# Kernel tuning notes

Measured on AMD Instinct MI355X. Metric: run time of the kernel, lower is better.

## Reference

```python
import jax, jax.numpy as jnp
import numpy as np

KS = 3
K3 = KS ** 3
NUM_K = 4
KM_ITERS = 10  # fixed Lloyd iterations (original runs to tolerance)


def _unfold3d(xp, d, h, w):
    # xp: [B, C, d+2, h+2, w+2] -> [B, C, d, h, w, 27]; kernel dims flattened as (k1,k2,k3)
    sl = [xp[:, :, i:i + d, j:j + h, l:l + w]
          for i in range(KS) for j in range(KS) for l in range(KS)]
    return jnp.stack(sl, axis=-1)


def _kmeans(pts):
    # pts: [N, C]. Deterministic init with first NUM_K points, fixed Lloyd iterations.
    cent0 = pts[:NUM_K]

    def assign(cent):
        d2 = (jnp.sum(pts * pts, -1, keepdims=True)
              - 2.0 * (pts @ cent.T) + jnp.sum(cent * cent, -1))  # [N, K]
        return jnp.argmin(d2, axis=-1)

    def step(cent, _):
        oh = jax.nn.one_hot(assign(cent), NUM_K, dtype=pts.dtype)  # [N, K]
        cnt = jnp.maximum(oh.sum(0), 1.0)
        cent = (oh.T @ pts) / cnt[:, None]
        return cent, None

    cent, _ = jax.lax.scan(step, cent0, None, length=KM_ITERS)
    return assign(cent), cent


def _mlp3(z, w1, b1, w2, b2, w3, b3):
    z = jax.nn.relu(z @ w1 + b1)
    z = jax.nn.relu(z @ w2 + b2)
    return z @ w3 + b3


def reference(x, proj_w, base_w, gk_w1, gk_b1, gk_w2, gk_b2, gk_w3, gk_b3,
              gb_w1, gb_b1, gb_w2, gb_b2, gb_w3, gb_b3, prelu_a):
    b, c, d, h, w = x.shape
    o = base_w.shape[0]
    n = d * h * w
    x_in = x
    # 1x1x1 input projection (no bias)
    xp = jnp.einsum('oi,bidhw->bodhw', proj_w, x)
    xp = jnp.pad(xp, ((0, 0), (0, 0), (1, 1), (1, 1), (1, 1)))
    patches = _unfold3d(xp, d, h, w)                                # [b,c,d,h,w,27]
    # mean_type 's': mean over kernel dims -> per-voxel channel summary
    x_mean = patches.mean(-1).reshape(b, c, n).transpose(0, 2, 1)   # [b,n,c]
    idx, cent = jax.vmap(_kmeans)(x_mean)                           # [b,n], [b,K,c]
    feat = cent.reshape(b, NUM_K * c)
    # per-cluster dynamic kernel gates in (0,1)
    w_i = jax.nn.sigmoid(_mlp3(feat, gk_w1, gk_b1, gk_w2, gk_b2, gk_w3, gk_b3))
    w_i = w_i.reshape(b, NUM_K, K3).transpose(1, 0, 2)[:, :, None, None, :]  # [K,b,1,1,27]
    weight = (w_i * base_w).reshape(NUM_K, b, o, c * K3)            # [K,b,o,c*27]
    bias = _mlp3(feat, gb_w1, gb_b1, gb_w2, gb_b2, gb_w3, gb_b3)
    bias = bias.reshape(b, NUM_K, o).transpose(1, 0, 2)[..., None]  # [K,b,o,1]
    # im2col: [b, c*27, n] with (c, k) channel-major flattening as in the torch rearrange
    xf = patches.reshape(b, c, n, K3).transpose(0, 1, 3, 2).reshape(b, c * K3, n)
    out = jnp.einsum('kbof,bfn->kbon', weight, xf) + bias           # [K,b,o,n]
    mask = jax.nn.one_hot(idx, NUM_K, dtype=out.dtype)              # [b,n,K]
    out = (out * mask.transpose(2, 0, 1)[:, :, None, :]).sum(0)     # [b,o,n]
    out = out.reshape(b, o, d, h, w)
    out = jnp.where(out >= 0, out, prelu_a * out)                   # PReLU (single param)
    return out + x_in


def setup_inputs():
    key = jax.random.key(0)
    ks = jax.random.split(key, 12)
    B, C, O, D = 1, 64, 64, 40
    inner, inner2 = 128, 64
    fin = C * NUM_K

    def lin(k, i, o_):
        s = 1.0 / np.sqrt(i)
        return jax.random.uniform(k, (i, o_), jnp.float32, -s, s)

    return {
        'x': jax.random.normal(ks[0], (B, C, D, D, D), jnp.float32),
        'proj_w': jax.random.normal(ks[1], (C, C), jnp.float32) / np.sqrt(C),
        'base_w': jax.random.normal(ks[2], (O, C, K3), jnp.float32) / np.sqrt(C * K3),
        'gk_w1': lin(ks[3], fin, inner), 'gk_b1': jnp.zeros((inner,), jnp.float32),
        'gk_w2': lin(ks[4], inner, inner), 'gk_b2': jnp.zeros((inner,), jnp.float32),
        'gk_w3': lin(ks[5], inner, K3 * NUM_K), 'gk_b3': jnp.zeros((K3 * NUM_K,), jnp.float32),
        'gb_w1': lin(ks[6], fin, inner2), 'gb_b1': jnp.zeros((inner2,), jnp.float32),
        'gb_w2': lin(ks[7], inner2, inner2), 'gb_b2': jnp.zeros((inner2,), jnp.float32),
        'gb_w3': lin(ks[8], inner2, O * NUM_K), 'gb_b3': jnp.zeros((O * NUM_K,), jnp.float32),
        'prelu_a': jnp.full((1,), 0.25, jnp.float32),
    }
```

## Files before the change

### kernel.cpp

```cpp
#include <hip/hip_runtime.h>
#include <math.h>

typedef short v8s __attribute__((ext_vector_type(8)));
typedef float v4f __attribute__((ext_vector_type(4)));

#define NVOX 64000
#define NPAD 74088
#define P2   1764
#define GSTR 592704
#define NCPY 32
#define ITST (NCPY*260)

__device__ __forceinline__ unsigned short bf16rne(float f){
  unsigned int u = __float_as_uint(f);
  u += 0x7FFFu + ((u >> 16) & 1u);
  return (unsigned short)(u >> 16);
}

__global__ __launch_bounds__(256) void proj_k(const float* __restrict__ x,
                                              const float* __restrict__ pw,
                                              float* __restrict__ xp,
                                              short* __restrict__ xpt){
  int tid = threadIdx.x;
  int m = (blockIdx.x >> 1) * 256 + tid;
  int half = blockIdx.x & 1;
  float xv[64];
#pragma unroll
  for (int i = 0; i < 64; i++) xv[i] = x[(size_t)i * NVOX + m];
  int d = m / 1600; int r = m - d * 1600; int h = r / 40; int w = r - h * 40;
  int p = ((d + 1) * 42 + (h + 1)) * 42 + (w + 1);
  const float4* pw4 = (const float4*)pw;
  for (int g8 = half * 4; g8 < half * 4 + 4; g8++){
    v8s pk;
#pragma unroll
    for (int j = 0; j < 8; j++){
      int co = g8 * 8 + j;
      float acc = 0.f;
#pragma unroll
      for (int q = 0; q < 16; q++){
        float4 pv = pw4[co * 16 + q];
        acc = fmaf(pv.x, xv[4*q+0], acc);
        acc = fmaf(pv.y, xv[4*q+1], acc);
        acc = fmaf(pv.z, xv[4*q+2], acc);
        acc = fmaf(pv.w, xv[4*q+3], acc);
      }
      xp[(size_t)co * NVOX + m] = acc;
      pk[j] = (short)bf16rne(acc);
    }
    *(v8s*)(xpt + (size_t)g8 * GSTR + (size_t)p * 8) = pk;
  }
}

__global__ __launch_bounds__(256) void boxwh_k(const float* __restrict__ in,
                                               float* __restrict__ out){
  __shared__ float s0[1600], s1[1600];
  size_t base = (size_t)blockIdx.x * 1600;
  int t = threadIdx.x;
  for (int e = t; e < 1600; e += 256) s0[e] = in[base + e];
  __syncthreads();
  for (int e = t; e < 1600; e += 256){
    int w = e % 40;
    float s = s0[e];
    if (w > 0)  s += s0[e - 1];
    if (w < 39) s += s0[e + 1];
    s1[e] = s;
  }
  __syncthreads();
  for (int e = t; e < 1600; e += 256){
    int h = e / 40;
    float s = s1[e];
    if (h > 0)  s += s1[e - 40];
    if (h < 39) s += s1[e + 40];
    out[base + e] = s;
  }
}
__global__ void boxd_k(const float* __restrict__ in, float* __restrict__ out){
  int g = blockIdx.x * 256 + threadIdx.x;
  int d = (g / 1600) % 40;
  float s = in[g];
  if (d > 0)  s += in[g - 1600];
  if (d < 39) s += in[g + 1600];
  out[g] = s * (1.f / 27.f);
}

__global__ __launch_bounds__(256) void transp_k(const float* __restrict__ in,
                                                float* __restrict__ out,
                                                float* __restrict__ km){
  __shared__ float tile[64][65];
  int t = threadIdx.x;
  int nb = blockIdx.x * 64;
  int l = t & 63, g = t >> 6;
  for (int cc = g; cc < 64; cc += 4)
    tile[cc][l] = in[(size_t)cc * NVOX + nb + l];
  __syncthreads();
  if (blockIdx.x == 0){
    km[t] = tile[t & 63][t >> 6];
    if (t < 4) km[256 + t] = 1.f;
  }
  for (int nn = g; nn < 64; nn += 4)
    out[(size_t)(nb + nn) * 64 + l] = tile[l][nn];
}

__global__ __launch_bounds__(256) void assign_k(const float* __restrict__ xmt,
                                                const float* __restrict__ kin,
                                                float* __restrict__ kout,
                                                int* __restrict__ idx, int mode){
  __shared__ float s_cent[256];
  __shared__ float s_cc[4];
  __shared__ float s_red[260];
  __shared__ float s_x[256 * 65];
  __shared__ int   s_kb[256];
  int t = threadIdx.x, lane = t & 63, wv = t >> 6;
  int n = blockIdx.x * 256 + t;
  {
    float sum = 0.f, cnt = 0.f;
#pragma unroll
    for (int s = 0; s < NCPY; s++){
      sum += kin[s * 260 + t];
      cnt += kin[s * 260 + 256 + (t >> 6)];
    }
    s_cent[t] = sum / fmaxf(cnt, 1.f);
  }
  for (int j = t; j < 260; j += 256) s_red[j] = 0.f;
  __syncthreads();
  if (t < 4){
    const float4* cc4 = (const float4*)(s_cent + t * 64);
    float s = 0.f;
#pragma unroll
    for (int q = 0; q < 16; q++){
      float4 v = cc4[q];
      s = fmaf(v.x, v.x, s); s = fmaf(v.y, v.y, s);
      s = fmaf(v.z, v.z, s); s = fmaf(v.w, v.w, s);
    }
    s_cc[t] = s;
  }
  __syncthreads();
  const float4* xt = (const float4*)(xmt + (size_t)n * 64);
  float4 xq[16];
#pragma unroll
  for (int q = 0; q < 16; q++) xq[q] = xt[q];
  float d0 = 0.f, d1 = 0.f, d2 = 0.f, d3 = 0.f;
  const float4* c4 = (const float4*)s_cent;
#pragma unroll
  for (int q = 0; q < 16; q++){
    float4 p0 = c4[q], p1 = c4[16 + q], p2 = c4[32 + q], p3 = c4[48 + q];
    d0 = fmaf(p0.x, xq[q].x, d0); d0 = fmaf(p0.y, xq[q].y, d0);
    d0 = fmaf(p0.z, xq[q].z, d0); d0 = fmaf(p0.w, xq[q].w, d0);
    d1 = fmaf(p1.x, xq[q].x, d1); d1 = fmaf(p1.y, xq[q].y, d1);
    d1 = fmaf(p1.z, xq[q].z, d1); d1 = fmaf(p1.w, xq[q].w, d1);
    d2 = fmaf(p2.x, xq[q].x, d2); d2 = fmaf(p2.y, xq[q].y, d2);
    d2 = fmaf(p2.z, xq[q].z, d2); d2 = fmaf(p2.w, xq[q].w, d2);
    d3 = fmaf(p3.x, xq[q].x, d3); d3 = fmaf(p3.y, xq[q].y, d3);
    d3 = fmaf(p3.z, xq[q].z, d3); d3 = fmaf(p3.w, xq[q].w, d3);
  }
  float sc0 = s_cc[0] - 2.f * d0;
  float sc1 = s_cc[1] - 2.f * d1;
  float sc2 = s_cc[2] - 2.f * d2;
  float sc3 = s_cc[3] - 2.f * d3;
  int kb = 0; float bs = sc0;
  if (sc1 < bs){ bs = sc1; kb = 1; }
  if (sc2 < bs){ bs = sc2; kb = 2; }
  if (sc3 < bs){ bs = sc3; kb = 3; }
  if (mode){
    idx[n] = kb;
    return;
  }
  s_kb[t] = kb;
#pragma unroll
  for (int q = 0; q < 16; q++){
    s_x[t * 65 + 4*q + 0] = xq[q].x;
    s_x[t * 65 + 4*q + 1] = xq[q].y;
    s_x[t * 65 + 4*q + 2] = xq[q].z;
    s_x[t * 65 + 4*q + 3] = xq[q].w;
  }
  __syncthreads();
  float a0 = 0.f, a1 = 0.f, a2 = 0.f, a3 = 0.f;
  int rowbase = wv * 64;
#pragma unroll 16
  for (int j = 0; j < 64; j++){
    float v = s_x[(rowbase + j) * 65 + lane];
    int kj = s_kb[rowbase + j];
    a0 += (kj == 0) ? v : 0.f;
    a1 += (kj == 1) ? v : 0.f;
    a2 += (kj == 2) ? v : 0.f;
    a3 += (kj == 3) ? v : 0.f;
  }
  atomicAdd(&s_red[lane], a0);
  atomicAdd(&s_red[64 + lane], a1);
  atomicAdd(&s_red[128 + lane], a2);
  atomicAdd(&s_red[192 + lane], a3);
#pragma unroll
  for (int kk = 0; kk < 4; kk++){
    unsigned long long m = __ballot(kb == kk);
    if (lane == 0) atomicAdd(&s_red[256 + kk], (float)__popcll(m));
  }
  __syncthreads();
  float* kslot = kout + (blockIdx.x & (NCPY - 1)) * 260;
  for (int j = t; j < 260; j += 256) atomicAdd(&kslot[j], s_red[j]);
}

__global__ void mlp_k(const float* __restrict__ km10,
                      const float* __restrict__ w1, const float* __restrict__ b1,
                      const float* __restrict__ w2, const float* __restrict__ b2,
                      const float* __restrict__ w3, const float* __restrict__ b3,
                      const float* __restrict__ u1, const float* __restrict__ c1,
                      const float* __restrict__ u2, const float* __restrict__ c2,
                      const float* __restrict__ u3, const float* __restrict__ c3,
                      float* __restrict__ wi, float* __restrict__ bias){
  __shared__ float s_feat[256], s_h1[128], s_h2[128], s_g1[64], s_g2[64];
  int t = threadIdx.x;
  {
    float sum = 0.f, cnt = 0.f;
#pragma unroll
    for (int s = 0; s < NCPY; s++){
      sum += km10[s * 260 + t];
      cnt += km10[s * 260 + 256 + (t >> 6)];
    }
    s_feat[t] = sum / fmaxf(cnt, 1.f);
  }
  __syncthreads();
  if (t < 128){
    float z = b1[t];
    for (int i = 0; i < 256; i++) z = fmaf(s_feat[i], w1[i * 128 + t], z);
    s_h1[t] = fmaxf(z, 0.f);
  }
  __syncthreads();
  if (t < 128){
    float z = b2[t];
    for (int i = 0; i < 128; i++) z = fmaf(s_h1[i], w2[i * 128 + t], z);
    s_h2[t] = fmaxf(z, 0.f);
  }
  __syncthreads();
  if (t < 108){
    float z = b3[t];
    for (int i = 0; i < 128; i++) z = fmaf(s_h2[i], w3[i * 108 + t], z);
    wi[t] = 1.f / (1.f + expf(-z));
  }
  if (t < 64){
    float z = c1[t];
    for (int i = 0; i < 256; i++) z = fmaf(s_feat[i], u1[i * 64 + t], z);
    s_g1[t] = fmaxf(z, 0.f);
  }
  __syncthreads();
  if (t < 64){
    float z = c2[t];
    for (int i = 0; i < 64; i++) z = fmaf(s_g1[i], u2[i * 64 + t], z);
    s_g2[t] = fmaxf(z, 0.f);
  }
  __syncthreads();
  {
    float z = c3[t];
    for (int i = 0; i < 64; i++) z = fmaf(s_g2[i], u3[i * 256 + t], z);
    bias[t] = z;
  }
}

__global__ void bwprep_k(const float* __restrict__ bw, short* __restrict__ bwb){
  int e = blockIdx.x * 256 + threadIdx.x;
  int t = e >> 12; int rem = e & 4095;
  int o = rem >> 6; int c = rem & 63;
  bwb[e] = (short)bf16rne(bw[(o * 64 + c) * 27 + t]);
}

__global__ __launch_bounds__(256) void conv_k(const short* __restrict__ xpt,
                                              const short* __restrict__ bwb,
                                              const float* __restrict__ wi,
                                              const float* __restrict__ bias,
                                              const int* __restrict__ idx,
                                              const float* __restrict__ x,
                                              const float* __restrict__ pa,
                                              float* __restrict__ out){
  static const int POFF[27] = {
    -P2-42-1, -P2-42, -P2-42+1, -P2-1, -P2, -P2+1, -P2+42-1, -P2+42, -P2+42+1,
    -42-1, -42, -42+1, -1, 0, 1, 42-1, 42, 42+1,
    P2-42-1, P2-42, P2-42+1, P2-1, P2, P2+1, P2+42-1, P2+42, P2+42+1 };
  __shared__ float s_wi[108];
  __shared__ float s_bias[256];
  __shared__ float s_acc[64 * 68];
  int tid = threadIdx.x;
  for (int j = tid; j < 108; j += 256) s_wi[j] = wi[j];
  s_bias[tid] = bias[tid];
  __syncthreads();
  int wv = tid >> 6, lane = tid & 63;
  int kc = wv & 1, mh = wv >> 1;
  int col = lane & 15, kg = lane >> 4;
  int vb = blockIdx.x * 64;
  int p4[4], ki4[4];
#pragma unroll
  for (int nt = 0; nt < 4; nt++){
    int v = vb + nt * 16 + col;
    ki4[nt] = idx[v];
    int d = v / 1600; int r = v - d * 1600; int h = r / 40; int w = r - h * 40;
    p4[nt] = ((d + 1) * 42 + (h + 1)) * 42 + (w + 1);
  }
  const short* bg = xpt + (size_t)(kc * 4 + kg) * GSTR;
  const short* bp0 = bg + (size_t)p4[0] * 8;
  const short* bp1 = bg + (size_t)p4[1] * 8;
  const short* bp2 = bg + (size_t)p4[2] * 8;
  const short* bp3 = bg + (size_t)p4[3] * 8;
  int ao0 = (mh * 32 + col) * 64 + kc * 32 + kg * 8;
  int ao1 = ao0 + 16 * 64;
  v4f acc[2][4];
#pragma unroll
  for (int m2 = 0; m2 < 2; m2++)
#pragma unroll
    for (int nt = 0; nt < 4; nt++) acc[m2][nt] = (v4f){0.f, 0.f, 0.f, 0.f};
  v4f zero = {0.f, 0.f, 0.f, 0.f};
#pragma unroll 9
  for (int t = 0; t < 27; t++){
    int po8 = POFF[t] * 8;
    v8s a0 = *(const v8s*)(bwb + t * 4096 + ao0);
    v8s a1 = *(const v8s*)(bwb + t * 4096 + ao1);
    v8s b0 = *(const v8s*)(bp0 + po8);
    v8s b1 = *(const v8s*)(bp1 + po8);
    v8s b2 = *(const v8s*)(bp2 + po8);
    v8s b3 = *(const v8s*)(bp3 + po8);
    float wk0 = s_wi[ki4[0] * 27 + t];
    float wk1 = s_wi[ki4[1] * 27 + t];
    float wk2 = s_wi[ki4[2] * 27 + t];
    float wk3 = s_wi[ki4[3] * 27 + t];
    v4f tp;
    tp = __builtin_amdgcn_mfma_f32_16x16x32_bf16(a0, b0, zero, 0, 0, 0); acc[0][0] += tp * wk0;
    tp = __builtin_amdgcn_mfma_f32_16x16x32_bf16(a1, b0, zero, 0, 0, 0); acc[1][0] += tp * wk0;
    tp = __builtin_amdgcn_mfma_f32_16x16x32_bf16(a0, b1, zero, 0, 0, 0); acc[0][1] += tp * wk1;
    tp = __builtin_amdgcn_mfma_f32_16x16x32_bf16(a1, b1, zero, 0, 0, 0); acc[1][1] += tp * wk1;
    tp = __builtin_amdgcn_mfma_f32_16x16x32_bf16(a0, b2, zero, 0, 0, 0); acc[0][2] += tp * wk2;
    tp = __builtin_amdgcn_mfma_f32_16x16x32_bf16(a1, b2, zero, 0, 0, 0); acc[1][2] += tp * wk2;
    tp = __builtin_amdgcn_mfma_f32_16x16x32_bf16(a0, b3, zero, 0, 0, 0); acc[0][3] += tp * wk3;
    tp = __builtin_amdgcn_mfma_f32_16x16x32_bf16(a1, b3, zero, 0, 0, 0); acc[1][3] += tp * wk3;
  }
  __syncthreads();
  if (kc == 1){
#pragma unroll
    for (int m2 = 0; m2 < 2; m2++)
#pragma unroll
      for (int nt = 0; nt < 4; nt++)
        *(v4f*)(&s_acc[(nt * 16 + col) * 68 + mh * 32 + m2 * 16 + kg * 4]) = acc[m2][nt];
  }
  __syncthreads();
  if (kc == 0){
    float pav = pa[0];
#pragma unroll
    for (int m2 = 0; m2 < 2; m2++){
#pragma unroll
      for (int nt = 0; nt < 4; nt++){
        v4f other = *(const v4f*)(&s_acc[(nt * 16 + col) * 68 + mh * 32 + m2 * 16 + kg * 4]);
        v4f sum = acc[m2][nt] + other;
        int n = vb + nt * 16 + col;
#pragma unroll
        for (int r = 0; r < 4; r++){
          int o = mh * 32 + m2 * 16 + kg * 4 + r;
          float val = sum[r] + s_bias[ki4[nt] * 64 + o];
          val = (val >= 0.f) ? val : pav * val;
          size_t off = (size_t)o * NVOX + n;
          out[off] = val + x[off];
        }
      }
    }
  }
}

extern "C" void kernel_launch(void* const* d_in, const int* in_sizes, int n_in,
                              void* d_out, int out_size, void* d_ws, size_t ws_size,
                              hipStream_t stream){
  const float* x    = (const float*)d_in[0];
  const float* pw   = (const float*)d_in[1];
  const float* bw   = (const float*)d_in[2];
  const float* gkw1 = (const float*)d_in[3];
  const float* gkb1 = (const float*)d_in[4];
  const float* gkw2 = (const float*)d_in[5];
  const float* gkb2 = (const float*)d_in[6];
  const float* gkw3 = (const float*)d_in[7];
  const float* gkb3 = (const float*)d_in[8];
  const float* gbw1 = (const float*)d_in[9];
  const float* gbb1 = (const float*)d_in[10];
  const float* gbw2 = (const float*)d_in[11];
  const float* gbb2 = (const float*)d_in[12];
  const float* gbw3 = (const float*)d_in[13];
  const float* gbb3 = (const float*)d_in[14];
  const float* pa   = (const float*)d_in[15];
  float* outp = (float*)d_out;

  float* ws   = (float*)d_ws;
  float* XP   = ws;
  float* BU2  = ws + 4096000;
  float* BU1  = ws + 8192000;
  short* XPT  = (short*)(ws + 12288000);
  short* BWB  = XPT + (size_t)NPAD * 64;
  float* KM   = (float*)(BWB + 110592);
  float* WI   = KM + 11 * ITST;
  float* BIAS = WI + 108;
  int*   IDX  = (int*)(BIAS + 256);
  float* XMT  = XP;

  hipMemsetAsync(XPT, 0, (size_t)NPAD * 64 * 2, stream);
  hipMemsetAsync(KM, 0, (size_t)11 * ITST * sizeof(float), stream);
  proj_k<<<500, 256, 0, stream>>>(x, pw, XP, XPT);
  boxwh_k<<<2560, 256, 0, stream>>>(XP, BU2);
  boxd_k<<<16000, 256, 0, stream>>>(BU2, BU1);
  transp_k<<<1000, 256, 0, stream>>>(BU1, XMT, KM);
  for (int i = 0; i <= 10; i++)
    assign_k<<<250, 256, 0, stream>>>(XMT, KM + i * ITST, KM + (i + 1) * ITST, IDX,
                                      (i == 10) ? 1 : 0);
  mlp_k<<<1, 256, 0, stream>>>(KM + 10 * ITST,
                               gkw1, gkb1, gkw2, gkb2, gkw3, gkb3,
                               gbw1, gbb1, gbw2, gbb2, gbw3, gbb3,
                               WI, BIAS);
  bwprep_k<<<432, 256, 0, stream>>>(bw, BWB);
  conv_k<<<1000, 256, 0, stream>>>(XPT, BWB, WI, BIAS, IDX, x, pa, outp);
}
```

Before: 322.5 us.

## Fuse k-means iterations into one persistent kernel with grid-wide barrier

Replaces the eleven separate assign_k launches with a single persistent kernel that loops over Lloyd iterations and synchronizes all 250 blocks via a two-level atomic counter barrier. Each block keeps its point data in registers and shared memory across iterations instead of reloading it every launch. This removes per-launch overhead and repeated global reads of the point matrix. It relies on all 250 blocks being co-resident and adds spin-wait barrier latency plus coherent loads of the partial sums.

```diff
diff --git a/kernel.cpp b/kernel.cpp
--- a/kernel.cpp
+++ b/kernel.cpp
@@ -15,6 +15,10 @@
   unsigned int u = __float_as_uint(f);
   u += 0x7FFFu + ((u >> 16) & 1u);
   return (unsigned short)(u >> 16);
+}
+
+__device__ __forceinline__ float cohload(const float* p){
+  return __hip_atomic_load(p, __ATOMIC_RELAXED, __HIP_MEMORY_SCOPE_AGENT);
 }
 
 __global__ __launch_bounds__(256) void proj_k(const float* __restrict__ x,
@@ -101,10 +105,11 @@
     out[(size_t)(nb + nn) * 64 + l] = tile[l][nn];
 }
 
-__global__ __launch_bounds__(256) void assign_k(const float* __restrict__ xmt,
-                                                const float* __restrict__ kin,
-                                                float* __restrict__ kout,
-                                                int* __restrict__ idx, int mode){
+__global__ __launch_bounds__(256) void kmeansp_k(const float* __restrict__ xmt,
+                                                 float* __restrict__ km,
+                                                 int* __restrict__ gcnt,
+                                                 int* __restrict__ gmast,
+                                                 int* __restrict__ idx){
   __shared__ float s_cent[256];
   __shared__ float s_cc[4];
   __shared__ float s_red[260];
@@ -112,60 +117,11 @@
   __shared__ int   s_kb[256];
   int t = threadIdx.x, lane = t & 63, wv = t >> 6;
   int n = blockIdx.x * 256 + t;
-  {
-    float sum = 0.f, cnt = 0.f;
-#pragma unroll
-    for (int s = 0; s < NCPY; s++){
-      sum += kin[s * 260 + t];
-      cnt += kin[s * 260 + 256 + (t >> 6)];
-    }
-    s_cent[t] = sum / fmaxf(cnt, 1.f);
-  }
-  for (int j = t; j < 260; j += 256) s_red[j] = 0.f;
-  __syncthreads();
-  if (t < 4){
-    const float4* cc4 = (const float4*)(s_cent + t * 64);
-    float s = 0.f;
-#pragma unroll
-    for (int q = 0; q < 16; q++){
-      float4 v = cc4[q];
-      s = fmaf(v.x, v.x, s); s = fmaf(v.y, v.y, s);
-      s = fmaf(v.z, v.z, s); s = fmaf(v.w, v.w, s);
-    }
-    s_cc[t] = s;
-  }
-  __syncthreads();
+
   const float4* xt = (const float4*)(xmt + (size_t)n * 64);
   float4 xq[16];
 #pragma unroll
   for (int q = 0; q < 16; q++) xq[q] = xt[q];
-  float d0 = 0.f, d1 = 0.f, d2 = 0.f, d3 = 0.f;
-  const float4* c4 = (const float4*)s_cent;
-#pragma unroll
-  for (int q = 0; q < 16; q++){
-    float4 p0 = c4[q], p1 = c4[16 + q], p2 = c4[32 + q], p3 = c4[48 + q];
-    d0 = fmaf(p0.x, xq[q].x, d0); d0 = fmaf(p0.y, xq[q].y, d0);
-    d0 = fmaf(p0.z, xq[q].z, d0); d0 = fmaf(p0.w, xq[q].w, d0);
-    d1 = fmaf(p1.x, xq[q].x, d1); d1 = fmaf(p1.y, xq[q].y, d1);
-    d1 = fmaf(p1.z, xq[q].z, d1); d1 = fmaf(p1.w, xq[q].w, d1);
-    d2 = fmaf(p2.x, xq[q].x, d2); d2 = fmaf(p2.y, xq[q].y, d2);
-    d2 = fmaf(p2.z, xq[q].z, d2); d2 = fmaf(p2.w, xq[q].w, d2);
-    d3 = fmaf(p3.x, xq[q].x, d3); d3 = fmaf(p3.y, xq[q].y, d3);
-    d3 = fmaf(p3.z, xq[q].z, d3); d3 = fmaf(p3.w, xq[q].w, d3);
-  }
-  float sc0 = s_cc[0] - 2.f * d0;
-  float sc1 = s_cc[1] - 2.f * d1;
-  float sc2 = s_cc[2] - 2.f * d2;
-  float sc3 = s_cc[3] - 2.f * d3;
-  int kb = 0; float bs = sc0;
-  if (sc1 < bs){ bs = sc1; kb = 1; }
-  if (sc2 < bs){ bs = sc2; kb = 2; }
-  if (sc3 < bs){ bs = sc3; kb = 3; }
-  if (mode){
-    idx[n] = kb;
-    return;
-  }
-  s_kb[t] = kb;
 #pragma unroll
   for (int q = 0; q < 16; q++){
     s_x[t * 65 + 4*q + 0] = xq[q].x;
@@ -173,30 +129,96 @@
     s_x[t * 65 + 4*q + 2] = xq[q].z;
     s_x[t * 65 + 4*q + 3] = xq[q].w;
   }
-  __syncthreads();
-  float a0 = 0.f, a1 = 0.f, a2 = 0.f, a3 = 0.f;
-  int rowbase = wv * 64;
+
+  for (int iter = 0; iter <= 10; ++iter){
+    const float* kin = km + iter * ITST;
+    {
+      float sum = 0.f, cnt = 0.f;
+#pragma unroll
+      for (int s = 0; s < NCPY; s++){
+        sum += cohload(&kin[s * 260 + t]);
+        cnt += cohload(&kin[s * 260 + 256 + (t >> 6)]);
+      }
+      s_cent[t] = sum / fmaxf(cnt, 1.f);
+    }
+    for (int j = t; j < 260; j += 256) s_red[j] = 0.f;
+    __syncthreads();
+    if (t < 4){
+      const float4* cc4 = (const float4*)(s_cent + t * 64);
+      float s = 0.f;
+#pragma unroll
+      for (int q = 0; q < 16; q++){
+        float4 v = cc4[q];
+        s = fmaf(v.x, v.x, s); s = fmaf(v.y, v.y, s);
+        s = fmaf(v.z, v.z, s); s = fmaf(v.w, v.w, s);
+      }
+      s_cc[t] = s;
+    }
+    __syncthreads();
+    float d0 = 0.f, d1 = 0.f, d2 = 0.f, d3 = 0.f;
+    const float4* c4 = (const float4*)s_cent;
+#pragma unroll
+    for (int q = 0; q < 16; q++){
+      float4 p0 = c4[q], p1 = c4[16 + q], p2 = c4[32 + q], p3 = c4[48 + q];
+      d0 = fmaf(p0.x, xq[q].x, d0); d0 = fmaf(p0.y, xq[q].y, d0);
+      d0 = fmaf(p0.z, xq[q].z, d0); d0 = fmaf(p0.w, xq[q].w, d0);
+      d1 = fmaf(p1.x, xq[q].x, d1); d1 = fmaf(p1.y, xq[q].y, d1);
+      d1 = fmaf(p1.z, xq[q].z, d1); d1 = fmaf(p1.w, xq[q].w, d1);
+      d2 = fmaf(p2.x, xq[q].x, d2); d2 = fmaf(p2.y, xq[q].y, d2);
+      d2 = fmaf(p2.z, xq[q].z, d2); d2 = fmaf(p2.w, xq[q].w, d2);
+      d3 = fmaf(p3.x, xq[q].x, d3); d3 = fmaf(p3.y, xq[q].y, d3);
+      d3 = fmaf(p3.z, xq[q].z, d3); d3 = fmaf(p3.w, xq[q].w, d3);
+    }
+    float sc0 = s_cc[0] - 2.f * d0;
+    float sc1 = s_cc[1] - 2.f * d1;
+    float sc2 = s_cc[2] - 2.f * d2;
+    float sc3 = s_cc[3] - 2.f * d3;
+    int kb = 0; float bs = sc0;
+    if (sc1 < bs){ bs = sc1; kb = 1; }
+    if (sc2 < bs){ bs = sc2; kb = 2; }
+    if (sc3 < bs){ bs = sc3; kb = 3; }
+    if (iter == 10){
+      idx[n] = kb;
+      return;
+    }
+    s_kb[t] = kb;
+    __syncthreads();
+    float a0 = 0.f, a1 = 0.f, a2 = 0.f, a3 = 0.f;
+    int rowbase = wv * 64;
 #pragma unroll 16
-  for (int j = 0; j < 64; j++){
-    float v = s_x[(rowbase + j) * 65 + lane];
-    int kj = s_kb[rowbase + j];
-    a0 += (kj == 0) ? v : 0.f;
-    a1 += (kj == 1) ? v : 0.f;
-    a2 += (kj == 2) ? v : 0.f;
-    a3 += (kj == 3) ? v : 0.f;
-  }
-  atomicAdd(&s_red[lane], a0);
-  atomicAdd(&s_red[64 + lane], a1);
-  atomicAdd(&s_red[128 + lane], a2);
-  atomicAdd(&s_red[192 + lane], a3);
-#pragma unroll
-  for (int kk = 0; kk < 4; kk++){
-    unsigned long long m = __ballot(kb == kk);
-    if (lane == 0) atomicAdd(&s_red[256 + kk], (float)__popcll(m));
-  }
-  __syncthreads();
-  float* kslot = kout + (blockIdx.x & (NCPY - 1)) * 260;
-  for (int j = t; j < 260; j += 256) atomicAdd(&kslot[j], s_red[j]);
+    for (int j = 0; j < 64; j++){
+      float v = s_x[(rowbase + j) * 65 + lane];
+      int kj = s_kb[rowbase + j];
+      a0 += (kj == 0) ? v : 0.f;
+      a1 += (kj == 1) ? v : 0.f;
+      a2 += (kj == 2) ? v : 0.f;
+      a3 += (kj == 3) ? v : 0.f;
+    }
+    atomicAdd(&s_red[lane], a0);
+    atomicAdd(&s_red[64 + lane], a1);
+    atomicAdd(&s_red[128 + lane], a2);
+    atomicAdd(&s_red[192 + lane], a3);
+#pragma unroll
+    for (int kk = 0; kk < 4; kk++){
+      unsigned long long m = __ballot(kb == kk);
+      if (lane == 0) atomicAdd(&s_red[256 + kk], (float)__popcll(m));
+    }
+    __syncthreads();
+    float* kslot = km + (iter + 1) * ITST + (blockIdx.x & 31) * 260;
+    for (int j = t; j < 260; j += 256) atomicAdd(&kslot[j], s_red[j]);
+    __threadfence();
+    __syncthreads();
+    if (t == 0){
+      int g = blockIdx.x & 31;
+      int gsz = (g < 26) ? 8 : 7;
+      if (atomicAdd(&gcnt[iter * 32 + g], 1) == gsz - 1)
+        atomicAdd(&gmast[iter], 1);
+      while (__hip_atomic_load(&gmast[iter], __ATOMIC_ACQUIRE,
+                               __HIP_MEMORY_SCOPE_AGENT) < 32)
+        __builtin_amdgcn_s_sleep(2);
+    }
+    __syncthreads();
+  }
 }
 
 __global__ void mlp_k(const float* __restrict__ km10,
@@ -388,20 +410,20 @@
   short* XPT  = (short*)(ws + 12288000);
   short* BWB  = XPT + (size_t)NPAD * 64;
   float* KM   = (float*)(BWB + 110592);
-  float* WI   = KM + 11 * ITST;
+  int*   GC   = (int*)(KM + 11 * ITST);
+  int*   GM   = GC + 11 * 32;
+  float* WI   = (float*)(GM + 16);
   float* BIAS = WI + 108;
   int*   IDX  = (int*)(BIAS + 256);
   float* XMT  = XP;
 
   hipMemsetAsync(XPT, 0, (size_t)NPAD * 64 * 2, stream);
-  hipMemsetAsync(KM, 0, (size_t)11 * ITST * sizeof(float), stream);
+  hipMemsetAsync(KM, 0, (size_t)(11 * ITST + 368) * 4, stream);
   proj_k<<<500, 256, 0, stream>>>(x, pw, XP, XPT);
   boxwh_k<<<2560, 256, 0, stream>>>(XP, BU2);
   boxd_k<<<16000, 256, 0, stream>>>(BU2, BU1);
   transp_k<<<1000, 256, 0, stream>>>(BU1, XMT, KM);
-  for (int i = 0; i <= 10; i++)
-    assign_k<<<250, 256, 0, stream>>>(XMT, KM + i * ITST, KM + (i + 1) * ITST, IDX,
-                                      (i == 10) ? 1 : 0);
+  kmeansp_k<<<250, 256, 0, stream>>>(XMT, KM, GC, GM, IDX);
   mlp_k<<<1, 256, 0, stream>>>(KM + 10 * ITST,
                                gkw1, gkb1, gkw2, gkb2, gkw3, gkb3,
                                gbw1, gbb1, gbw2, gbb2, gbw3, gbb3,
```

Result: slower. 618.3 us (+91.7%).

## Fold memsets, weight prep and MLP into existing kernels to cut launches

Applied to the files above, without the earlier changes.

The two memsets and the bf16 weight-prep kernel are folded into a single prep kernel with block-role dispatch. That kernel zeroes only the halo of the padded bf16 buffer, and the projection now uses quarters rather than halves for more blocks. The KM zeroing moves into the transpose kernel, and the gate/bias MLP runs in block 0 of the final assign launch using the centroids already in shared memory. This removes several launches and a full-buffer memset. In exchange, assign_k carries more shared memory and the MLP is serialized inside one block. It also relies on transp_k zeroing KM before the next assign reads it.

```diff
diff --git a/kernel.cpp b/kernel.cpp
--- a/kernel.cpp
+++ b/kernel.cpp
@@ -17,37 +17,57 @@
   return (unsigned short)(u >> 16);
 }
 
-__global__ __launch_bounds__(256) void proj_k(const float* __restrict__ x,
+__global__ __launch_bounds__(256) void prep_k(const float* __restrict__ x,
                                               const float* __restrict__ pw,
                                               float* __restrict__ xp,
-                                              short* __restrict__ xpt){
+                                              short* __restrict__ xpt,
+                                              const float* __restrict__ bw,
+                                              short* __restrict__ bwb){
   int tid = threadIdx.x;
-  int m = (blockIdx.x >> 1) * 256 + tid;
-  int half = blockIdx.x & 1;
-  float xv[64];
-#pragma unroll
-  for (int i = 0; i < 64; i++) xv[i] = x[(size_t)i * NVOX + m];
-  int d = m / 1600; int r = m - d * 1600; int h = r / 40; int w = r - h * 40;
-  int p = ((d + 1) * 42 + (h + 1)) * 42 + (w + 1);
-  const float4* pw4 = (const float4*)pw;
-  for (int g8 = half * 4; g8 < half * 4 + 4; g8++){
-    v8s pk;
-#pragma unroll
-    for (int j = 0; j < 8; j++){
-      int co = g8 * 8 + j;
-      float acc = 0.f;
-#pragma unroll
-      for (int q = 0; q < 16; q++){
-        float4 pv = pw4[co * 16 + q];
-        acc = fmaf(pv.x, xv[4*q+0], acc);
-        acc = fmaf(pv.y, xv[4*q+1], acc);
-        acc = fmaf(pv.z, xv[4*q+2], acc);
-        acc = fmaf(pv.w, xv[4*q+3], acc);
-      }
-      xp[(size_t)co * NVOX + m] = acc;
-      pk[j] = (short)bf16rne(acc);
-    }
-    *(v8s*)(xpt + (size_t)g8 * GSTR + (size_t)p * 8) = pk;
+  int bid = blockIdx.x;
+  if (bid < 1000){
+    int m = (bid >> 2) * 256 + tid;
+    int quarter = bid & 3;
+    float xv[64];
+#pragma unroll
+    for (int i = 0; i < 64; i++) xv[i] = x[(size_t)i * NVOX + m];
+    int d = m / 1600; int r = m - d * 1600; int h = r / 40; int w = r - h * 40;
+    int p = ((d + 1) * 42 + (h + 1)) * 42 + (w + 1);
+    const float4* pw4 = (const float4*)pw;
+    for (int g8 = quarter * 2; g8 < quarter * 2 + 2; g8++){
+      v8s pk;
+#pragma unroll
+      for (int j = 0; j < 8; j++){
+        int co = g8 * 8 + j;
+        float acc = 0.f;
+#pragma unroll
+        for (int q = 0; q < 16; q++){
+          float4 pv = pw4[co * 16 + q];
+          acc = fmaf(pv.x, xv[4*q+0], acc);
+          acc = fmaf(pv.y, xv[4*q+1], acc);
+          acc = fmaf(pv.z, xv[4*q+2], acc);
+          acc = fmaf(pv.w, xv[4*q+3], acc);
+        }
+        xp[(size_t)co * NVOX + m] = acc;
+        pk[j] = (short)bf16rne(acc);
+      }
+      *(v8s*)(xpt + (size_t)g8 * GSTR + (size_t)p * 8) = pk;
+    }
+  } else if (bid < 1432){
+    int e = (bid - 1000) * 256 + tid;
+    int t5 = e >> 12; int rem = e & 4095;
+    int o = rem >> 6; int c = rem & 63;
+    bwb[e] = (short)bf16rne(bw[(o * 64 + c) * 27 + t5]);
+  } else {
+    v8s z = (v8s){0,0,0,0,0,0,0,0};
+    for (int p = (bid - 1432) * 256 + tid; p < NPAD; p += 40 * 256){
+      int d = p / P2; int rem = p - d * P2; int h = rem / 42; int w = rem - h * 42;
+      if (d == 0 || d == 41 || h == 0 || h == 41 || w == 0 || w == 41){
+#pragma unroll
+        for (int g = 0; g < 8; g++)
+          *(v8s*)(xpt + (size_t)g * GSTR + (size_t)p * 8) = z;
+      }
+    }
   }
 }
 
@@ -90,6 +110,8 @@
   int t = threadIdx.x;
   int nb = blockIdx.x * 64;
   int l = t & 63, g = t >> 6;
+  for (int j = 260 + blockIdx.x * 256 + t; j < 11 * ITST; j += 1000 * 256)
+    km[j] = 0.f;
   for (int cc = g; cc < 64; cc += 4)
     tile[cc][l] = in[(size_t)cc * NVOX + nb + l];
   __syncthreads();
@@ -104,12 +126,20 @@
 __global__ __launch_bounds__(256) void assign_k(const float* __restrict__ xmt,
                                                 const float* __restrict__ kin,
                                                 float* __restrict__ kout,
-                                                int* __restrict__ idx, int mode){
+                                                int* __restrict__ idx, int mode,
+                      const float* __restrict__ w1, const float* __restrict__ b1,
+                      const float* __restrict__ w2, const float* __restrict__ b2,
+                      const float* __restrict__ w3, const float* __restrict__ b3,
+                      const float* __restrict__ u1, const float* __restrict__ c1,
+                      const float* __restrict__ u2, const float* __restrict__ c2,
+                      const float* __restrict__ u3, const float* __restrict__ c3,
+                      float* __restrict__ wi, float* __restrict__ bias){
   __shared__ float s_cent[256];
   __shared__ float s_cc[4];
   __shared__ float s_red[260];
   __shared__ float s_x[256 * 65];
   __shared__ int   s_kb[256];
+  __shared__ float s_h1[128], s_h2[128], s_g1[64], s_g2[64];
   int t = threadIdx.x, lane = t & 63, wv = t >> 6;
   int n = blockIdx.x * 256 + t;
   {
@@ -163,6 +193,41 @@
   if (sc3 < bs){ bs = sc3; kb = 3; }
   if (mode){
     idx[n] = kb;
+    if (blockIdx.x == 0){
+      __syncthreads();
+      if (t < 128){
+        float z = b1[t];
+        for (int i = 0; i < 256; i++) z = fmaf(s_cent[i], w1[i * 128 + t], z);
+        s_h1[t] = fmaxf(z, 0.f);
+      }
+      if (t < 64){
+        float z = c1[t];
+        for (int i = 0; i < 256; i++) z = fmaf(s_cent[i], u1[i * 64 + t], z);
+        s_g1[t] = fmaxf(z, 0.f);
+      }
+      __syncthreads();
+      if (t < 128){
+        float z = b2[t];
+        for (int i = 0; i < 128; i++) z = fmaf(s_h1[i], w2[i * 128 + t], z);
+        s_h2[t] = fmaxf(z, 0.f);
+      }
+      if (t < 64){
+        float z = c2[t];
+        for (int i = 0; i < 64; i++) z = fmaf(s_g1[i], u2[i * 64 + t], z);
+        s_g2[t] = fmaxf(z, 0.f);
+      }
+      __syncthreads();
+      if (t < 108){
+        float z = b3[t];
+        for (int i = 0; i < 128; i++) z = fmaf(s_h2[i], w3[i * 108 + t], z);
+        wi[t] = 1.f / (1.f + expf(-z));
+      }
+      {
+        float z = c3[t];
+        for (int i = 0; i < 64; i++) z = fmaf(s_g2[i], u3[i * 256 + t], z);
+        bias[t] = z;
+      }
+    }
     return;
   }
   s_kb[t] = kb;
@@ -197,69 +262,6 @@
   __syncthreads();
   float* kslot = kout + (blockIdx.x & (NCPY - 1)) * 260;
   for (int j = t; j < 260; j += 256) atomicAdd(&kslot[j], s_red[j]);
-}
-
-__global__ void mlp_k(const float* __restrict__ km10,
-                      const float* __restrict__ w1, const float* __restrict__ b1,
-                      const float* __restrict__ w2, const float* __restrict__ b2,
-                      const float* __restrict__ w3, const float* __restrict__ b3,
-                      const float* __restrict__ u1, const float* __restrict__ c1,
-                      const float* __restrict__ u2, const float* __restrict__ c2,
-                      const float* __restrict__ u3, const float* __restrict__ c3,
-                      float* __restrict__ wi, float* __restrict__ bias){
-  __shared__ float s_feat[256], s_h1[128], s_h2[128], s_g1[64], s_g2[64];
-  int t = threadIdx.x;
-  {
-    float sum = 0.f, cnt = 0.f;
-#pragma unroll
-    for (int s = 0; s < NCPY; s++){
-      sum += km10[s * 260 + t];
-      cnt += km10[s * 260 + 256 + (t >> 6)];
-    }
-    s_feat[t] = sum / fmaxf(cnt, 1.f);
-  }
-  __syncthreads();
-  if (t < 128){
-    float z = b1[t];
-    for (int i = 0; i < 256; i++) z = fmaf(s_feat[i], w1[i * 128 + t], z);
-    s_h1[t] = fmaxf(z, 0.f);
-  }
-  __syncthreads();
-  if (t < 128){
-    float z = b2[t];
-    for (int i = 0; i < 128; i++) z = fmaf(s_h1[i], w2[i * 128 + t], z);
-    s_h2[t] = fmaxf(z, 0.f);
-  }
-  __syncthreads();
-  if (t < 108){
-    float z = b3[t];
-    for (int i = 0; i < 128; i++) z = fmaf(s_h2[i], w3[i * 108 + t], z);
-    wi[t] = 1.f / (1.f + expf(-z));
-  }
-  if (t < 64){
-    float z = c1[t];
-    for (int i = 0; i < 256; i++) z = fmaf(s_feat[i], u1[i * 64 + t], z);
-    s_g1[t] = fmaxf(z, 0.f);
-  }
-  __syncthreads();
-  if (t < 64){
-    float z = c2[t];
-    for (int i = 0; i < 64; i++) z = fmaf(s_g1[i], u2[i * 64 + t], z);
-    s_g2[t] = fmaxf(z, 0.f);
-  }
-  __syncthreads();
-  {
-    float z = c3[t];
-    for (int i = 0; i < 64; i++) z = fmaf(s_g2[i], u3[i * 256 + t], z);
-    bias[t] = z;
-  }
-}
-
-__global__ void bwprep_k(const float* __restrict__ bw, short* __restrict__ bwb){
-  int e = blockIdx.x * 256 + threadIdx.x;
-  int t = e >> 12; int rem = e & 4095;
-  int o = rem >> 6; int c = rem & 63;
-  bwb[e] = (short)bf16rne(bw[(o * 64 + c) * 27 + t]);
 }
 
 __global__ __launch_bounds__(256) void conv_k(const short* __restrict__ xpt,
@@ -393,19 +395,15 @@
   int*   IDX  = (int*)(BIAS + 256);
   float* XMT  = XP;
 
-  hipMemsetAsync(XPT, 0, (size_t)NPAD * 64 * 2, stream);
-  hipMemsetAsync(KM, 0, (size_t)11 * ITST * sizeof(float), stream);
-  proj_k<<<500, 256, 0, stream>>>(x, pw, XP, XPT);
+  prep_k<<<1472, 256, 0, stream>>>(x, pw, XP, XPT, bw, BWB);
   boxwh_k<<<2560, 256, 0, stream>>>(XP, BU2);
   boxd_k<<<16000, 256, 0, stream>>>(BU2, BU1);
   transp_k<<<1000, 256, 0, stream>>>(BU1, XMT, KM);
   for (int i = 0; i <= 10; i++)
     assign_k<<<250, 256, 0, stream>>>(XMT, KM + i * ITST, KM + (i + 1) * ITST, IDX,
-                                      (i == 10) ? 1 : 0);
-  mlp_k<<<1, 256, 0, stream>>>(KM + 10 * ITST,
-                               gkw1, gkb1, gkw2, gkb2, gkw3, gkb3,
-                               gbw1, gbb1, gbw2, gbb2, gbw3, gbb3,
-                               WI, BIAS);
-  bwprep_k<<<432, 256, 0, stream>>>(bw, BWB);
+                                      (i == 10) ? 1 : 0,
+                                      gkw1, gkb1, gkw2, gkb2, gkw3, gkb3,
+                                      gbw1, gbb1, gbw2, gbb2, gbw3, gbb3,
+                                      WI, BIAS);
   conv_k<<<1000, 256, 0, stream>>>(XPT, BWB, WI, BIAS, IDX, x, pa, outp);
 }
```

Result: faster. 310.1 us (-3.8%).
